# Performance work log

Hardware: AMD Instinct MI355X
Metric: run time of the kernel (lower is better)

The kernel has to match this reference:

```python
import jax, jax.numpy as jnp
import numpy as np

SIGMA = 1.0  # isotropic Gaussian bandwidth (init kwarg)


def setup_inputs() -> dict:
    key = jax.random.key(0)
    X = jax.random.normal(key, (16384, 64), dtype=jnp.float32)
    return {"X": X}


def reference(X):
    # pairwise squared distances: ||x_i||^2 - 2 x_i.x_j + ||x_j||^2
    sumX2 = jnp.sum(X * X, axis=1, keepdims=True)          # [n, 1]
    D2 = sumX2 - 2.0 * (X @ X.T) + sumX2.T                  # [n, n]
    D2 = jnp.maximum(D2, 0.0)
    K = jnp.exp(-D2 / (2.0 * SIGMA ** 2))
    return K
```

## Files before the change

### kernel.cpp

```cpp
#include <hip/hip_runtime.h>
#include <stdint.h>


typedef __attribute__((ext_vector_type(8))) short s16x8;
typedef __attribute__((ext_vector_type(4))) float f32x4;

#define DDIM 64
#define JT 8
#define LROW 36
#define LOG2E      1.4426950408889634f
#define HALF_LOG2E 0.7213475204444817f

__device__ inline short cvt1(float x, float& sq) {
  uint32_t u = __builtin_bit_cast(uint32_t, x);
  uint32_t r = (u + 0x7fffu + ((u >> 16) & 1u)) & 0xffff0000u;
  float hf = __builtin_bit_cast(float, r);
  sq += hf * hf;
  return (short)(r >> 16);
}

__device__ inline void issue_row(const float* __restrict__ X, int row, int lq,
                                 f32x4 r[4]) {
  const f32x4* p = reinterpret_cast<const f32x4*>(X + (size_t)row * DDIM + lq * 8);
  const f32x4* q = reinterpret_cast<const f32x4*>(X + (size_t)row * DDIM + 32 + lq * 8);
  r[0] = p[0]; r[1] = p[1]; r[2] = q[0]; r[3] = q[1];
}

__device__ inline void cvt_row(const f32x4 r[4], s16x8 h[2], float& hnorm) {
  float s = 0.f;
#pragma unroll
  for (int ks = 0; ks < 2; ++ks) {
    s16x8 hh;
    hh[0] = cvt1(r[2*ks][0], s);   hh[1] = cvt1(r[2*ks][1], s);
    hh[2] = cvt1(r[2*ks][2], s);   hh[3] = cvt1(r[2*ks][3], s);
    hh[4] = cvt1(r[2*ks+1][0], s); hh[5] = cvt1(r[2*ks+1][1], s);
    hh[6] = cvt1(r[2*ks+1][2], s); hh[7] = cvt1(r[2*ks+1][3], s);
    h[ks] = hh;
  }
  s += __shfl_xor(s, 16);
  s += __shfl_xor(s, 32);
  hnorm = -HALF_LOG2E * s;
}

__global__ __launch_bounds__(256, 2) void gauss_gram_kernel(
    const float* __restrict__ X, float* __restrict__ K, int n) {
  const int lane = threadIdx.x & 63;
  const int wid  = threadIdx.x >> 6;
  const int wr = wid >> 1;
  const int wc = wid & 1;
  const int l15 = lane & 15;
  const int lq  = lane >> 4;
  const int r8  = lane >> 3;
  const int e8  = lane & 7;

  __shared__ float tbuf[4][64 * LROW];
  float* buf = tbuf[wid];

  const int i0     = blockIdx.x * 128 + wr * 64;
  const int jstrip = blockIdx.y * (128 * JT);

  f32x4 araw[4][4];
#pragma unroll
  for (int mi = 0; mi < 4; ++mi)
    issue_row(X, i0 + mi * 16 + l15, lq, araw[mi]);

  f32x4 braw[4][4];
#pragma unroll
  for (int ni = 0; ni < 4; ++ni)
    issue_row(X, jstrip + wc * 64 + ni * 16 + l15, lq, braw[ni]);

  s16x8 a[4][2]; float hA[4];
#pragma unroll
  for (int mi = 0; mi < 4; ++mi)
    cvt_row(araw[mi], a[mi], hA[mi]);

#pragma unroll
  for (int jt = 0; jt < JT; ++jt) {
    const int j0 = jstrip + jt * 128 + wc * 64;

    s16x8 b[4][2]; float hcol[4][4];
#pragma unroll
    for (int ni = 0; ni < 4; ++ni) {
      float hB;
      cvt_row(braw[ni], b[ni], hB);
#pragma unroll
      for (int r = 0; r < 4; ++r)
        hcol[ni][r] = __shfl(hB, lq * 4 + r);
    }

    if (jt + 1 < JT) {
#pragma unroll
      for (int ni = 0; ni < 4; ++ni)
        issue_row(X, jstrip + (jt + 1) * 128 + wc * 64 + ni * 16 + l15, lq, braw[ni]);
    }
    __builtin_amdgcn_sched_barrier(0x1 | 0x2 | 0x4 | 0x8);

    f32x4 acc[4][4] = {};
#pragma unroll
    for (int ks = 0; ks < 2; ++ks)
#pragma unroll
      for (int mi = 0; mi < 4; ++mi)
#pragma unroll
        for (int ni = 0; ni < 4; ++ni)
          acc[mi][ni] = __builtin_amdgcn_mfma_f32_16x16x32_bf16(
              b[ni][ks], a[mi][ks], acc[mi][ni], 0, 0, 0);

#pragma unroll
    for (int half = 0; half < 2; ++half) {
#pragma unroll
      for (int mi = 0; mi < 4; ++mi) {
        const int rg = i0 + mi * 16 + l15;
#pragma unroll
        for (int nh = 0; nh < 2; ++nh) {
          const int ni = half * 2 + nh;
          const int c0 = j0 + ni * 16 + lq * 4;
          f32x4 v;
#pragma unroll
          for (int r = 0; r < 4; ++r) {
            float arg = fminf(hA[mi] + hcol[ni][r] + LOG2E * acc[mi][ni][r], 0.0f);
            float e = exp2f(arg);
            v[r] = (rg == c0 + r) ? 1.0f : e;
          }
          *reinterpret_cast<f32x4*>(
              buf + (mi * 16 + l15) * LROW + nh * 16 + lq * 4) = v;
        }
      }
#pragma unroll
      for (int g = 0; g < 8; ++g) {
        f32x4 t = *reinterpret_cast<const f32x4*>(
            buf + (g * 8 + r8) * LROW + e8 * 4);
        const int rg = i0 + g * 8 + r8;
        *reinterpret_cast<f32x4*>(
            K + (size_t)rg * n + j0 + half * 32 + e8 * 4) = t;
      }
    }
  }
}

extern "C" void kernel_launch(void* const* d_in, const int* in_sizes, int n_in,
                              void* d_out, int out_size, void* d_ws, size_t ws_size,
                              hipStream_t stream) {
  (void)n_in; (void)d_ws; (void)ws_size; (void)out_size;
  const float* X = (const float*)d_in[0];
  float* K = (float*)d_out;
  const int n = in_sizes[0] / DDIM;
  dim3 grid(n / 128, n / (128 * JT));
  gauss_gram_kernel<<<grid, 256, 0, stream>>>(X, K, n);
}
```

Baseline: 224.4 us.

## Halve per-wave column tile, raise occupancy, skip diagonal check off-diagonal

Shrinks each wave's column tile from 64 to 32, halving accumulators, B-operand registers and LDS staging, and raises launch bounds to three blocks per CU with twice as many blocks in y. The epilogue only does the diagonal compare on tiles that intersect the diagonal, and drops the clamp of the exponent argument to zero. The aim is more waves in flight to hide the store-bound output traffic. In exchange, the A rows are reloaded for twice as many blocks, and without the clamp near-duplicate points could produce values slightly above one.

```diff
diff --git a/kernel.cpp b/kernel.cpp
--- a/kernel.cpp
+++ b/kernel.cpp
@@ -42,7 +42,7 @@
   hnorm = -HALF_LOG2E * s;
 }
 
-__global__ __launch_bounds__(256, 2) void gauss_gram_kernel(
+__global__ __launch_bounds__(256, 3) void gauss_gram_kernel(
     const float* __restrict__ X, float* __restrict__ K, int n) {
   const int lane = threadIdx.x & 63;
   const int wid  = threadIdx.x >> 6;
@@ -53,21 +53,22 @@
   const int r8  = lane >> 3;
   const int e8  = lane & 7;
 
-  __shared__ float tbuf[4][64 * LROW];
+  __shared__ float tbuf[4][32 * LROW];
   float* buf = tbuf[wid];
 
   const int i0     = blockIdx.x * 128 + wr * 64;
-  const int jstrip = blockIdx.y * (128 * JT);
+  const int jstrip = blockIdx.y * (64 * JT);
+  const int jw     = wc * 32;
 
   f32x4 araw[4][4];
 #pragma unroll
   for (int mi = 0; mi < 4; ++mi)
     issue_row(X, i0 + mi * 16 + l15, lq, araw[mi]);
 
-  f32x4 braw[4][4];
+  f32x4 braw[2][4];
 #pragma unroll
-  for (int ni = 0; ni < 4; ++ni)
-    issue_row(X, jstrip + wc * 64 + ni * 16 + l15, lq, braw[ni]);
+  for (int ni = 0; ni < 2; ++ni)
+    issue_row(X, jstrip + jw + ni * 16 + l15, lq, braw[ni]);
 
   s16x8 a[4][2]; float hA[4];
 #pragma unroll
@@ -76,11 +77,11 @@
 
 #pragma unroll
   for (int jt = 0; jt < JT; ++jt) {
-    const int j0 = jstrip + jt * 128 + wc * 64;
+    const int j0 = jstrip + jt * 64 + jw;
 
-    s16x8 b[4][2]; float hcol[4][4];
+    s16x8 b[2][2]; float hcol[2][4];
 #pragma unroll
-    for (int ni = 0; ni < 4; ++ni) {
+    for (int ni = 0; ni < 2; ++ni) {
       float hB;
       cvt_row(braw[ni], b[ni], hB);
 #pragma unroll
@@ -90,48 +91,57 @@
 
     if (jt + 1 < JT) {
 #pragma unroll
-      for (int ni = 0; ni < 4; ++ni)
-        issue_row(X, jstrip + (jt + 1) * 128 + wc * 64 + ni * 16 + l15, lq, braw[ni]);
+      for (int ni = 0; ni < 2; ++ni)
+        issue_row(X, jstrip + (jt + 1) * 64 + jw + ni * 16 + l15, lq, braw[ni]);
     }
     __builtin_amdgcn_sched_barrier(0x1 | 0x2 | 0x4 | 0x8);
 
-    f32x4 acc[4][4] = {};
+    f32x4 acc[4][2] = {};
 #pragma unroll
     for (int ks = 0; ks < 2; ++ks)
 #pragma unroll
       for (int mi = 0; mi < 4; ++mi)
 #pragma unroll
-        for (int ni = 0; ni < 4; ++ni)
+        for (int ni = 0; ni < 2; ++ni)
           acc[mi][ni] = __builtin_amdgcn_mfma_f32_16x16x32_bf16(
               b[ni][ks], a[mi][ks], acc[mi][ni], 0, 0, 0);
 
+    const bool diag = (i0 < j0 + 32) && (j0 < i0 + 64);
+
 #pragma unroll
-    for (int half = 0; half < 2; ++half) {
+    for (int p = 0; p < 2; ++p) {
 #pragma unroll
-      for (int mi = 0; mi < 4; ++mi) {
+      for (int mh = 0; mh < 2; ++mh) {
+        const int mi = p * 2 + mh;
         const int rg = i0 + mi * 16 + l15;
 #pragma unroll
-        for (int nh = 0; nh < 2; ++nh) {
-          const int ni = half * 2 + nh;
+        for (int ni = 0; ni < 2; ++ni) {
           const int c0 = j0 + ni * 16 + lq * 4;
           f32x4 v;
+          if (diag) {
 #pragma unroll
-          for (int r = 0; r < 4; ++r) {
-            float arg = fminf(hA[mi] + hcol[ni][r] + LOG2E * acc[mi][ni][r], 0.0f);
-            float e = exp2f(arg);
-            v[r] = (rg == c0 + r) ? 1.0f : e;
+            for (int r = 0; r < 4; ++r) {
+              float arg = hA[mi] + hcol[ni][r] + LOG2E * acc[mi][ni][r];
+              float e = exp2f(arg);
+              v[r] = (rg == c0 + r) ? 1.0f : e;
+            }
+          } else {
+#pragma unroll
+            for (int r = 0; r < 4; ++r) {
+              float arg = hA[mi] + hcol[ni][r] + LOG2E * acc[mi][ni][r];
+              v[r] = exp2f(arg);
+            }
           }
           *reinterpret_cast<f32x4*>(
-              buf + (mi * 16 + l15) * LROW + nh * 16 + lq * 4) = v;
+              buf + (mh * 16 + l15) * LROW + ni * 16 + lq * 4) = v;
         }
       }
 #pragma unroll
-      for (int g = 0; g < 8; ++g) {
+      for (int g = 0; g < 4; ++g) {
         f32x4 t = *reinterpret_cast<const f32x4*>(
             buf + (g * 8 + r8) * LROW + e8 * 4);
-        const int rg = i0 + g * 8 + r8;
-        *reinterpret_cast<f32x4*>(
-            K + (size_t)rg * n + j0 + half * 32 + e8 * 4) = t;
+        const int rg = i0 + p * 32 + g * 8 + r8;
+        *reinterpret_cast<f32x4*>(K + (size_t)rg * n + j0 + e8 * 4) = t;
       }
     }
   }
@@ -144,6 +154,6 @@
   const float* X = (const float*)d_in[0];
   float* K = (float*)d_out;
   const int n = in_sizes[0] / DDIM;
-  dim3 grid(n / 128, n / (128 * JT));
+  dim3 grid(n / 128, n / (64 * JT));
   gauss_gram_kernel<<<grid, 256, 0, stream>>>(X, K, n);
 }
```

Result: slower. 265.8 us (+18.4%).
